# Kernel tuning notes

Hardware: AMD Instinct MI355X
Metric: run time of the kernel (lower is better)

Reference implementation:

```python
import jax, jax.numpy as jnp
import numpy as np

N = 200000
E = 6400000
IN_F = 128
HID = 128
OUT_F = 16
LAYERS = 3
EPS = 1e-5


def setup_inputs() -> dict:
    key = jax.random.key(0)
    ks = jax.random.split(key, 12)
    nodes = jax.random.normal(ks[0], (N, IN_F), dtype=jnp.float32)
    src = jax.random.randint(ks[1], (E,), 0, N, dtype=jnp.int32)
    dst = jax.random.randint(ks[2], (E,), 0, N, dtype=jnp.int32)
    s_in = 1.0 / np.sqrt(IN_F)
    s_h = 1.0 / np.sqrt(HID)
    W_in = jax.random.uniform(ks[3], (IN_F, HID), jnp.float32, -s_in, s_in)
    b_in = jax.random.uniform(ks[4], (HID,), jnp.float32, -s_in, s_in)
    Ws = jax.random.uniform(ks[5], (LAYERS, HID, HID), jnp.float32, -s_h, s_h)
    bs = jax.random.uniform(ks[6], (LAYERS, HID), jnp.float32, -s_h, s_h)
    gammas = jnp.ones((LAYERS, HID), jnp.float32)
    betas = jnp.zeros((LAYERS, HID), jnp.float32)
    W_out = jax.random.uniform(ks[7], (HID, OUT_F), jnp.float32, -s_h, s_h)
    b_out = jax.random.uniform(ks[8], (OUT_F,), jnp.float32, -s_h, s_h)
    return {"nodes": nodes, "src": src, "dst": dst, "W_in": W_in, "b_in": b_in,
            "Ws": Ws, "bs": bs, "gammas": gammas, "betas": betas,
            "W_out": W_out, "b_out": b_out}


def _layernorm(x, g, b):
    mu = jnp.mean(x, axis=-1, keepdims=True)
    var = jnp.var(x, axis=-1, keepdims=True)
    return (x - mu) * jax.lax.rsqrt(var + EPS) * g + b


def reference(nodes, src, dst, W_in, b_in, Ws, bs, gammas, betas, W_out, b_out):
    # in-degree for 'gcn' aggregator normalization: (sum_neigh + self) / (deg + 1)
    deg = jax.ops.segment_sum(jnp.ones((E,), jnp.float32), dst, num_segments=N)
    inv = 1.0 / (deg + 1.0)  # [N]
    x = nodes @ W_in + b_in  # [N, HID]
    for l in range(LAYERS):
        agg = jax.ops.segment_sum(x[src], dst, num_segments=N)  # gather+scatter-add
        h = (agg + x) * inv[:, None]          # gcn mean incl. self
        h = h @ Ws[l] + bs[l]                 # fc_neigh
        h = jax.nn.relu(h)                    # activation (before norm, per DGL)
        x = _layernorm(h, gammas[l], betas[l])
    return x @ W_out + b_out  # [N, OUT_F]
```

## Files before the change

kernel.cpp:

```cpp
#include <hip/hip_runtime.h>

#define N_NODES 200000
#define N_EDGES 6400000
#define HID 128
#define OUTF 16
#define LAYERS 3
#define EPS 1e-5f

#define NRANGES 16
#define RANGE_N 12500
#define NBUCKETS 800
#define BUCKET_N 250
#define BATCH 5000
#define NBATCH (N_EDGES / BATCH)
#define RCAP 405000
#define RBLK (RCAP / BATCH)
#define BCAP 9500

typedef unsigned int u32;

__device__ __forceinline__ unsigned short f2bf(float f){
  unsigned int u = __float_as_uint(f);
  u += 0x7fffu + ((u >> 16) & 1u);
  return (unsigned short)(u >> 16);
}
__device__ __forceinline__ u32 pack2bf(float lo, float hi){
  return (u32)f2bf(lo) | ((u32)f2bf(hi) << 16);
}


__global__ __launch_bounds__(256) void k_initcur(int* __restrict__ range_cursor,
                                                 int* __restrict__ bucket_cursor){
  int t = blockIdx.x * 256 + threadIdx.x;
  if (t < NRANGES) range_cursor[t] = t * RCAP;
  if (t < NBUCKETS) bucket_cursor[t] = t * BCAP;
}


__global__ __launch_bounds__(256) void k_p1(const int* __restrict__ src, const int* __restrict__ dst,
                                            int* __restrict__ range_cursor, u32* __restrict__ ebuf1){
  __shared__ u32 stage[BATCH];
  __shared__ int hist[NRANGES], hist2[NRANGES], hbase[NRANGES], gbase[NRANGES];
  const int tid = threadIdx.x;
  const long e0 = (long)blockIdx.x * BATCH;

  if (tid < NRANGES){ hist[tid] = 0; hist2[tid] = 0; }
  __syncthreads();
  for (int i = tid; i < BATCH; i += 256){
    int d = dst[e0 + i];
    atomicAdd(&hist[d / RANGE_N], 1);
  }
  __syncthreads();
  if (tid == 0){ int run = 0; for (int b = 0; b < NRANGES; b++){ hbase[b] = run; run += hist[b]; } }
  __syncthreads();
  if (tid < NRANGES && hist[tid] > 0) gbase[tid] = atomicAdd(&range_cursor[tid], hist[tid]);
  __syncthreads();
  for (int i = tid; i < BATCH; i += 256){
    int d = dst[e0 + i];
    int s = src[e0 + i];
    int r = d / RANGE_N;
    u32 pk = ((u32)(d - r * RANGE_N) << 18) | (u32)s;
    int p = atomicAdd(&hist2[r], 1);
    stage[hbase[r] + p] = pk;
  }
  __syncthreads();
  for (int b = 0; b < NRANGES; b++){
    int len = hist[b];
    int gb = gbase[b], hb = hbase[b];
    for (int i = tid; i < len; i += 256) ebuf1[gb + i] = stage[hb + i];
  }
}


__global__ __launch_bounds__(256) void k_p2(const u32* __restrict__ ebuf1, const int* __restrict__ range_cursor,
                                            int* __restrict__ bucket_cursor, u32* __restrict__ ebuf2){
  __shared__ u32 stage[BATCH];
  __shared__ int hist[50], hist2[50], hbase[50], gbase[50];
  const int tid = threadIdx.x;
  const int r = blockIdx.x / RBLK;
  const int chunk = blockIdx.x % RBLK;
  const int rlen = range_cursor[r] - r * RCAP;
  const int i0 = chunk * BATCH;
  const int len = min(BATCH, rlen - i0);
  if (len <= 0) return;
  const u32* seg = ebuf1 + (long)r * RCAP + i0;

  if (tid < 50){ hist[tid] = 0; hist2[tid] = 0; }
  __syncthreads();
  for (int i = tid; i < len; i += 256){
    int dl = (int)(seg[i] >> 18);
    atomicAdd(&hist[dl / BUCKET_N], 1);
  }
  __syncthreads();
  if (tid == 0){ int run = 0; for (int b = 0; b < 50; b++){ hbase[b] = run; run += hist[b]; } }
  __syncthreads();
  if (tid < 50 && hist[tid] > 0) gbase[tid] = atomicAdd(&bucket_cursor[r * 50 + tid], hist[tid]);
  __syncthreads();
  for (int i = tid; i < len; i += 256){
    u32 pk = seg[i];
    int b = (int)(pk >> 18) / BUCKET_N;
    int p = atomicAdd(&hist2[b], 1);
    stage[hbase[b] + p] = pk;
  }
  __syncthreads();
  for (int b = 0; b < 50; b++){
    int l = hist[b];
    if (l == 0) continue;
    int gb = gbase[b], hb = hbase[b];
    for (int i = tid; i < l; i += 256) ebuf2[gb + i] = stage[hb + i];
  }
}


__global__ __launch_bounds__(256) void k_scanb(const int* __restrict__ bucket_cursor,
                                               int* __restrict__ bucket_base){
  __shared__ int q[256];
  int tid = threadIdx.x;
  int v[4]; int sum4 = 0;
  if (tid < 200){
    #pragma unroll
    for (int j = 0; j < 4; j++){ int b = 4 * tid + j; v[j] = bucket_cursor[b] - b * BCAP; sum4 += v[j]; }
  }
  q[tid] = sum4; __syncthreads();
  for (int off = 1; off < 256; off <<= 1){
    int t = (tid >= off) ? q[tid - off] : 0;
    __syncthreads();
    q[tid] += t;
    __syncthreads();
  }
  if (tid < 200){
    int run = q[tid] - sum4;
    #pragma unroll
    for (int j = 0; j < 4; j++){ bucket_base[4 * tid + j] = run; run += v[j]; }
  }
}


__global__ __launch_bounds__(256) void k_p3(const u32* __restrict__ ebuf2, const int* __restrict__ bucket_cursor,
                                            const int* __restrict__ bucket_base,
                                            int* __restrict__ csr, int* __restrict__ row_start){
  __shared__ int stage[BCAP];
  __shared__ int hist[BUCKET_N], sbase[BUCKET_N], cur[BUCKET_N];
  __shared__ int q[256];
  const int tid = threadIdx.x;
  const int b = blockIdx.x;
  const int n0 = b * BUCKET_N;
  const int dl0 = (b % 50) * BUCKET_N;
  const int len = min(bucket_cursor[b] - b * BCAP, BCAP);
  const int base = bucket_base[b];
  const u32* seg = ebuf2 + (long)b * BCAP;

  if (tid < BUCKET_N){ hist[tid] = 0; cur[tid] = 0; }
  __syncthreads();
  for (int i = tid; i < len; i += 256){
    int local = (int)(seg[i] >> 18) - dl0;
    local = min(max(local, 0), BUCKET_N - 1);
    atomicAdd(&hist[local], 1);
  }
  __syncthreads();
  {
    int v = (tid < BUCKET_N) ? hist[tid] : 0;
    q[tid] = v; __syncthreads();
    for (int off = 1; off < 256; off <<= 1){
      int t = (tid >= off) ? q[tid - off] : 0;
      __syncthreads();
      q[tid] += t;
      __syncthreads();
    }
    if (tid < BUCKET_N) sbase[tid] = q[tid] - v;
  }
  __syncthreads();
  for (int i = tid; i < len; i += 256){
    u32 pk = seg[i];
    int local = (int)(pk >> 18) - dl0;
    local = min(max(local, 0), BUCKET_N - 1);
    int pos = atomicAdd(&cur[local], 1);
    stage[sbase[local] + pos] = (int)(pk & 0x3FFFFu);
  }
  __syncthreads();
  for (int i = tid; i < len; i += 256) csr[base + i] = stage[i];
  if (tid < BUCKET_N) row_start[n0 + tid] = base + sbase[tid];
  if (b == NBUCKETS - 1 && tid == 0) row_start[N_NODES] = base + len;
}


__global__ __launch_bounds__(256) void k_gemm128(const float* __restrict__ A,
    const float* __restrict__ W, const float* __restrict__ bias,
    const float* __restrict__ gamma, const float* __restrict__ beta,
    float* __restrict__ xout, u32* __restrict__ xbout, int relu_ln)
{
  __shared__ float As[64][132];
  __shared__ float part[64][4][2];
  __shared__ float mu_s[64], rs_s[64];
  __shared__ float gam_s[128], bet_s[128];
  const int tid = threadIdx.x;
  const long row0 = (long)blockIdx.x * 64;

  const float4* A4 = (const float4*)(A + row0 * HID);
  for (int i = tid; i < 64 * 32; i += 256){
    int r = i >> 5, c = i & 31;
    *(float4*)&As[r][c * 4] = A4[r * 32 + c];
  }
  if (relu_ln && tid < 128){ gam_s[tid] = gamma[tid]; bet_s[tid] = beta[tid]; }
  __syncthreads();

  const int cg = tid & 31;
  const int rg = tid >> 5;
  const int c0 = cg * 4;
  float acc[8][4];
  {
    float4 b = *(const float4*)&bias[c0];
    #pragma unroll
    for (int r = 0; r < 8; r++){ acc[r][0]=b.x; acc[r][1]=b.y; acc[r][2]=b.z; acc[r][3]=b.w; }
  }

  for (int k = 0; k < HID; k += 4){
    float4 w0 = *(const float4*)&W[(k + 0) * HID + c0];
    float4 w1 = *(const float4*)&W[(k + 1) * HID + c0];
    float4 w2 = *(const float4*)&W[(k + 2) * HID + c0];
    float4 w3 = *(const float4*)&W[(k + 3) * HID + c0];
    #pragma unroll
    for (int r = 0; r < 8; r++){
      float4 a = *(const float4*)&As[rg * 8 + r][k];
      acc[r][0] = fmaf(a.w, w3.x, fmaf(a.z, w2.x, fmaf(a.y, w1.x, fmaf(a.x, w0.x, acc[r][0]))));
      acc[r][1] = fmaf(a.w, w3.y, fmaf(a.z, w2.y, fmaf(a.y, w1.y, fmaf(a.x, w0.y, acc[r][1]))));
      acc[r][2] = fmaf(a.w, w3.z, fmaf(a.z, w2.z, fmaf(a.y, w1.z, fmaf(a.x, w0.z, acc[r][2]))));
      acc[r][3] = fmaf(a.w, w3.w, fmaf(a.z, w2.w, fmaf(a.y, w1.w, fmaf(a.x, w0.w, acc[r][3]))));
    }
  }

  if (!relu_ln){
    #pragma unroll
    for (int r = 0; r < 8; r++){
      long row = row0 + rg * 8 + r;
      float4 v; v.x = acc[r][0]; v.y = acc[r][1]; v.z = acc[r][2]; v.w = acc[r][3];
      *(float4*)&xout[row * HID + c0] = v;
      uint2 p; p.x = pack2bf(v.x, v.y); p.y = pack2bf(v.z, v.w);
      *(uint2*)&xbout[(row * HID + c0) >> 1] = p;
    }
  } else {
    __syncthreads();
    #pragma unroll
    for (int r = 0; r < 8; r++){
      float4 v;
      v.x = fmaxf(acc[r][0], 0.f); v.y = fmaxf(acc[r][1], 0.f);
      v.z = fmaxf(acc[r][2], 0.f); v.w = fmaxf(acc[r][3], 0.f);
      *(float4*)&As[rg * 8 + r][c0] = v;
    }
    __syncthreads();
    {
      int row = tid >> 2, qq = tid & 3;
      float s = 0.f, s2 = 0.f;
      #pragma unroll 8
      for (int c = 0; c < 32; c++){ float v = As[row][qq * 32 + c]; s += v; s2 += v * v; }
      part[row][qq][0] = s; part[row][qq][1] = s2;
    }
    __syncthreads();
    if (tid < 64){
      float s  = part[tid][0][0] + part[tid][1][0] + part[tid][2][0] + part[tid][3][0];
      float s2 = part[tid][0][1] + part[tid][1][1] + part[tid][2][1] + part[tid][3][1];
      float mu = s * (1.f / HID);
      float var = s2 * (1.f / HID) - mu * mu;
      mu_s[tid] = mu;
      rs_s[tid] = 1.f / sqrtf(var + EPS);
    }
    __syncthreads();
    for (int i = tid; i < 64 * 32; i += 256){
      int r = i >> 5, c4 = (i & 31) * 4;
      float4 v = *(float4*)&As[r][c4];
      float mu = mu_s[r], rs = rs_s[r];
      v.x = (v.x - mu) * rs * gam_s[c4 + 0] + bet_s[c4 + 0];
      v.y = (v.y - mu) * rs * gam_s[c4 + 1] + bet_s[c4 + 1];
      v.z = (v.z - mu) * rs * gam_s[c4 + 2] + bet_s[c4 + 2];
      v.w = (v.w - mu) * rs * gam_s[c4 + 3] + bet_s[c4 + 3];
      long row = row0 + r;
      *(float4*)&xout[row * HID + c4] = v;
      uint2 p; p.x = pack2bf(v.x, v.y); p.y = pack2bf(v.z, v.w);
      *(uint2*)&xbout[(row * HID + c4) >> 1] = p;
    }
  }
}


typedef float f32x2_t __attribute__((ext_vector_type(2)));

__global__ __launch_bounds__(256) void k_agg(const int* __restrict__ row_start, const int* __restrict__ csr,
    const uint2* __restrict__ xb2, const float* __restrict__ x, float* __restrict__ h)
{
  int gid  = blockIdx.x * 256 + threadIdx.x;
  int node = gid >> 6;
  int lane = gid & 63;
  int half = lane >> 5, col = lane & 31;
  int s0 = row_start[node], s1 = row_start[node + 1];
  const uint2* xbc = xb2 + col;

  float4 xs = {0.f, 0.f, 0.f, 0.f};
  if (half == 0) xs = *(const float4*)&x[(long)node * HID + col * 4];

  f32x2_t a01 = {0.f, 0.f};
  f32x2_t a23 = {0.f, 0.f};

  int base = s0;
  int idx[8];
  if (base + 16 <= s1){
    #pragma unroll
    for (int j = 0; j < 8; j++) idx[j] = csr[base + 2*j + half];
  }
  while (base + 16 <= s1){
    uint2 p[8];
    #pragma unroll
    for (int j = 0; j < 8; j++) p[j] = xbc[(long)idx[j] * 32];
    base += 16;
    if (base + 16 <= s1){
      #pragma unroll
      for (int j = 0; j < 8; j++) idx[j] = csr[base + 2*j + half];
    }
    #pragma unroll
    for (int j = 0; j < 8; j++){
      f32x2_t v01 = { __uint_as_float(p[j].x << 16), __uint_as_float(p[j].x & 0xffff0000u) };
      f32x2_t v23 = { __uint_as_float(p[j].y << 16), __uint_as_float(p[j].y & 0xffff0000u) };
      a01 += v01;
      a23 += v23;
    }
  }
  if (base < s1){
    const int s1m1 = s1 - 1;
    int ti[8];
    #pragma unroll
    for (int j = 0; j < 8; j++) ti[j] = csr[min(base + 2*j + half, s1m1)];
    uint2 p[8];
    #pragma unroll
    for (int j = 0; j < 8; j++) p[j] = xbc[(long)ti[j] * 32];
    #pragma unroll
    for (int j = 0; j < 8; j++){
      bool act = (base + 2*j + half) < s1;
      float v0 = __uint_as_float(p[j].x << 16);
      float v1 = __uint_as_float(p[j].x & 0xffff0000u);
      float v2 = __uint_as_float(p[j].y << 16);
      float v3 = __uint_as_float(p[j].y & 0xffff0000u);
      a01.x += act ? v0 : 0.f;
      a01.y += act ? v1 : 0.f;
      a23.x += act ? v2 : 0.f;
      a23.y += act ? v3 : 0.f;
    }
  }

  float a0 = a01.x, a1 = a01.y, a2 = a23.x, a3 = a23.y;
  a0 += __shfl_down(a0, 32);
  a1 += __shfl_down(a1, 32);
  a2 += __shfl_down(a2, 32);
  a3 += __shfl_down(a3, 32);

  if (half == 0){
    float inv = 1.f / (float)(s1 - s0 + 1);
    long bidx = (long)node * HID + col * 4;
    float4 r;
    r.x = (a0 + xs.x) * inv;
    r.y = (a1 + xs.y) * inv;
    r.z = (a2 + xs.z) * inv;
    r.w = (a3 + xs.w) * inv;
    *(float4*)&h[bidx] = r;
  }
}


__global__ __launch_bounds__(256) void k_gemm_out(const float* __restrict__ x,
    const float* __restrict__ Wo, const float* __restrict__ bo, float* __restrict__ out)
{
  __shared__ float As[16][132];
  __shared__ float Wl[HID * OUTF];
  const int tid = threadIdx.x;
  const long row0 = (long)blockIdx.x * 16;
  const float4* A4 = (const float4*)(x + row0 * HID);
  for (int i = tid; i < 16 * 32; i += 256){
    int r = i >> 5, c = i & 31;
    *(float4*)&As[r][c * 4] = A4[r * 32 + c];
  }
  for (int i = tid; i < HID * OUTF; i += 256) Wl[i] = Wo[i];
  __syncthreads();
  int col = tid & 15, r = tid >> 4;
  float acc = bo[col];
  for (int k = 0; k < HID; k += 4){
    float4 a = *(const float4*)&As[r][k];
    acc = fmaf(a.x, Wl[(k + 0) * OUTF + col],
          fmaf(a.y, Wl[(k + 1) * OUTF + col],
          fmaf(a.z, Wl[(k + 2) * OUTF + col],
          fmaf(a.w, Wl[(k + 3) * OUTF + col], acc))));
  }
  out[(row0 + r) * OUTF + col] = acc;
}


extern "C" void kernel_launch(void* const* d_in, const int* in_sizes, int n_in,
                              void* d_out, int out_size, void* d_ws, size_t ws_size,
                              hipStream_t stream)
{
  (void)in_sizes; (void)n_in; (void)out_size; (void)ws_size;
  const float* nodes = (const float*)d_in[0];
  const int*   src   = (const int*)d_in[1];
  const int*   dst   = (const int*)d_in[2];
  const float* W_in  = (const float*)d_in[3];
  const float* b_in  = (const float*)d_in[4];
  const float* Ws    = (const float*)d_in[5];
  const float* bs    = (const float*)d_in[6];
  const float* gam   = (const float*)d_in[7];
  const float* bet   = (const float*)d_in[8];
  const float* W_out = (const float*)d_in[9];
  const float* b_out = (const float*)d_in[10];
  float* out = (float*)d_out;

  size_t off = 0;
  auto bump = [&](size_t bytes) -> char* {
    char* p = (char*)d_ws + off;
    off = (off + bytes + 255) & ~(size_t)255;
    return p;
  };
  int* row_start     = (int*)bump((N_NODES + 1) * sizeof(int));
  int* range_cursor  = (int*)bump(NRANGES * sizeof(int));
  int* bucket_cursor = (int*)bump(NBUCKETS * sizeof(int));
  int* bucket_base   = (int*)bump((NBUCKETS + 1) * sizeof(int));
  int* csr           = (int*)bump((size_t)N_EDGES * sizeof(int));
  float* x           = (float*)bump((size_t)N_NODES * HID * sizeof(float));
  float* h           = (float*)bump((size_t)N_NODES * HID * sizeof(float));
  u32* xb            = (u32*)bump((size_t)N_NODES * HID * sizeof(unsigned short));

  u32* ebuf1 = (u32*)x;
  u32* ebuf2 = (u32*)h;

  k_initcur<<<4, 256, 0, stream>>>(range_cursor, bucket_cursor);
  k_p1<<<NBATCH, 256, 0, stream>>>(src, dst, range_cursor, ebuf1);
  k_p2<<<NRANGES * RBLK, 256, 0, stream>>>(ebuf1, range_cursor, bucket_cursor, ebuf2);
  k_scanb<<<1, 256, 0, stream>>>(bucket_cursor, bucket_base);
  k_p3<<<NBUCKETS, 256, 0, stream>>>(ebuf2, bucket_cursor, bucket_base, csr, row_start);

  k_gemm128<<<N_NODES / 64, 256, 0, stream>>>(nodes, W_in, b_in, nullptr, nullptr, x, xb, 0);
  for (int l = 0; l < LAYERS; l++){
    k_agg<<<N_NODES / 4, 256, 0, stream>>>(row_start, csr, (const uint2*)xb, x, h);
    k_gemm128<<<N_NODES / 64, 256, 0, stream>>>(h, Ws + (size_t)l * HID * HID, bs + l * HID,
                                                gam + l * HID, bet + l * HID, x, xb, 1);
  }
  k_gemm_out<<<N_NODES / 16, 256, 0, stream>>>(x, W_out, b_out, out);
}
```

Measured before the change: 1.422 ms.

## Fuse neighbor aggregation into per-layer GEMM+ReLU+LayerNorm kernel with ping-pong buffers

Aggregation of bf16 neighbor features is performed inside the layer GEMM kernel, writing the normalized mean into shared memory instead of a global h buffer. This removes the write and re-read of the full intermediate activation tensor and one launch per layer. Because blocks read the previous layer's features while writing new ones, x and its bf16 copy are double-buffered. The trade-off is fewer, longer blocks where each wave processes 16 nodes sequentially, reducing gather parallelism and latency hiding.

```diff
diff --git a/kernel.cpp b/kernel.cpp
--- a/kernel.cpp
+++ b/kernel.cpp
@@ -186,13 +186,9 @@
 
 __global__ __launch_bounds__(256) void k_gemm128(const float* __restrict__ A,
     const float* __restrict__ W, const float* __restrict__ bias,
-    const float* __restrict__ gamma, const float* __restrict__ beta,
-    float* __restrict__ xout, u32* __restrict__ xbout, int relu_ln)
+    float* __restrict__ xout, u32* __restrict__ xbout)
 {
   __shared__ float As[64][132];
-  __shared__ float part[64][4][2];
-  __shared__ float mu_s[64], rs_s[64];
-  __shared__ float gam_s[128], bet_s[128];
   const int tid = threadIdx.x;
   const long row0 = (long)blockIdx.x * 64;
 
@@ -201,7 +197,6 @@
     int r = i >> 5, c = i & 31;
     *(float4*)&As[r][c * 4] = A4[r * 32 + c];
   }
-  if (relu_ln && tid < 128){ gam_s[tid] = gamma[tid]; bet_s[tid] = beta[tid]; }
   __syncthreads();
 
   const int cg = tid & 31;
@@ -229,137 +224,174 @@
     }
   }
 
-  if (!relu_ln){
+  #pragma unroll
+  for (int r = 0; r < 8; r++){
+    long row = row0 + rg * 8 + r;
+    float4 v; v.x = acc[r][0]; v.y = acc[r][1]; v.z = acc[r][2]; v.w = acc[r][3];
+    *(float4*)&xout[row * HID + c0] = v;
+    uint2 p; p.x = pack2bf(v.x, v.y); p.y = pack2bf(v.z, v.w);
+    *(uint2*)&xbout[(row * HID + c0) >> 1] = p;
+  }
+}
+
+
+__global__ __launch_bounds__(256) void k_fused(const int* __restrict__ row_start,
+    const int* __restrict__ csr, const uint2* __restrict__ xb2,
+    const float* __restrict__ x_old,
+    const float* __restrict__ W, const float* __restrict__ bias,
+    const float* __restrict__ gamma, const float* __restrict__ beta,
+    float* __restrict__ xout, u32* __restrict__ xbout)
+{
+  __shared__ float As[64][132];
+  __shared__ float part[64][4][2];
+  __shared__ float mu_s[64], rs_s[64];
+  __shared__ float gam_s[128], bet_s[128];
+  const int tid = threadIdx.x;
+  const long row0 = (long)blockIdx.x * 64;
+
+  if (tid < 128){ gam_s[tid] = gamma[tid]; bet_s[tid] = beta[tid]; }
+
+  {
+    const int wv = tid >> 6;
+    const int lane = tid & 63;
+    const int half = lane >> 5, col = lane & 31;
+    const uint2* xbc = xb2 + col;
+
+    for (int i = 0; i < 16; i++){
+      const int r = wv * 16 + i;
+      const int node = (int)row0 + r;
+      const int s0 = row_start[node], s1 = row_start[node + 1];
+
+      float4 xs = {0.f, 0.f, 0.f, 0.f};
+      if (half == 0) xs = *(const float4*)&x_old[(long)node * HID + col * 4];
+
+      float a0 = 0.f, a1 = 0.f, a2 = 0.f, a3 = 0.f;
+      int base = s0;
+      int idx[8];
+      if (base + 16 <= s1){
+        #pragma unroll
+        for (int j = 0; j < 8; j++) idx[j] = csr[base + 2*j + half];
+      }
+      while (base + 16 <= s1){
+        uint2 p[8];
+        #pragma unroll
+        for (int j = 0; j < 8; j++) p[j] = xbc[(long)idx[j] * 32];
+        base += 16;
+        if (base + 16 <= s1){
+          #pragma unroll
+          for (int j = 0; j < 8; j++) idx[j] = csr[base + 2*j + half];
+        }
+        #pragma unroll
+        for (int j = 0; j < 8; j++){
+          a0 += __uint_as_float(p[j].x << 16);
+          a1 += __uint_as_float(p[j].x & 0xffff0000u);
+          a2 += __uint_as_float(p[j].y << 16);
+          a3 += __uint_as_float(p[j].y & 0xffff0000u);
+        }
+      }
+      if (base < s1){
+        const int s1m1 = s1 - 1;
+        int ti[8];
+        #pragma unroll
+        for (int j = 0; j < 8; j++) ti[j] = csr[min(base + 2*j + half, s1m1)];
+        uint2 p[8];
+        #pragma unroll
+        for (int j = 0; j < 8; j++) p[j] = xbc[(long)ti[j] * 32];
+        #pragma unroll
+        for (int j = 0; j < 8; j++){
+          bool act = (base + 2*j + half) < s1;
+          float v0 = __uint_as_float(p[j].x << 16);
+          float v1 = __uint_as_float(p[j].x & 0xffff0000u);
+          float v2 = __uint_as_float(p[j].y << 16);
+          float v3 = __uint_as_float(p[j].y & 0xffff0000u);
+          a0 += act ? v0 : 0.f;
+          a1 += act ? v1 : 0.f;
+          a2 += act ? v2 : 0.f;
+          a3 += act ? v3 : 0.f;
+        }
+      }
+
+      a0 += __shfl_down(a0, 32);
+      a1 += __shfl_down(a1, 32);
+      a2 += __shfl_down(a2, 32);
+      a3 += __shfl_down(a3, 32);
+
+      if (half == 0){
+        float inv = 1.f / (float)(s1 - s0 + 1);
+        float4 rv;
+        rv.x = (a0 + xs.x) * inv;
+        rv.y = (a1 + xs.y) * inv;
+        rv.z = (a2 + xs.z) * inv;
+        rv.w = (a3 + xs.w) * inv;
+        *(float4*)&As[r][col * 4] = rv;
+      }
+    }
+  }
+  __syncthreads();
+
+  const int cg = tid & 31;
+  const int rg = tid >> 5;
+  const int c0 = cg * 4;
+  float acc[8][4];
+  {
+    float4 b = *(const float4*)&bias[c0];
+    #pragma unroll
+    for (int r = 0; r < 8; r++){ acc[r][0]=b.x; acc[r][1]=b.y; acc[r][2]=b.z; acc[r][3]=b.w; }
+  }
+
+  for (int k = 0; k < HID; k += 4){
+    float4 w0 = *(const float4*)&W[(k + 0) * HID + c0];
+    float4 w1 = *(const float4*)&W[(k + 1) * HID + c0];
+    float4 w2 = *(const float4*)&W[(k + 2) * HID + c0];
+    float4 w3 = *(const float4*)&W[(k + 3) * HID + c0];
     #pragma unroll
     for (int r = 0; r < 8; r++){
-      long row = row0 + rg * 8 + r;
-      float4 v; v.x = acc[r][0]; v.y = acc[r][1]; v.z = acc[r][2]; v.w = acc[r][3];
-      *(float4*)&xout[row * HID + c0] = v;
-      uint2 p; p.x = pack2bf(v.x, v.y); p.y = pack2bf(v.z, v.w);
-      *(uint2*)&xbout[(row * HID + c0) >> 1] = p;
+      float4 a = *(const float4*)&As[rg * 8 + r][k];
+      acc[r][0] = fmaf(a.w, w3.x, fmaf(a.z, w2.x, fmaf(a.y, w1.x, fmaf(a.x, w0.x, acc[r][0]))));
+      acc[r][1] = fmaf(a.w, w3.y, fmaf(a.z, w2.y, fmaf(a.y, w1.y, fmaf(a.x, w0.y, acc[r][1]))));
+      acc[r][2] = fmaf(a.w, w3.z, fmaf(a.z, w2.z, fmaf(a.y, w1.z, fmaf(a.x, w0.z, acc[r][2]))));
+      acc[r][3] = fmaf(a.w, w3.w, fmaf(a.z, w2.w, fmaf(a.y, w1.w, fmaf(a.x, w0.w, acc[r][3]))));
     }
-  } else {
-    __syncthreads();
-    #pragma unroll
-    for (int r = 0; r < 8; r++){
-      float4 v;
-      v.x = fmaxf(acc[r][0], 0.f); v.y = fmaxf(acc[r][1], 0.f);
-      v.z = fmaxf(acc[r][2], 0.f); v.w = fmaxf(acc[r][3], 0.f);
-      *(float4*)&As[rg * 8 + r][c0] = v;
-    }
-    __syncthreads();
-    {
-      int row = tid >> 2, qq = tid & 3;
-      float s = 0.f, s2 = 0.f;
-      #pragma unroll 8
-      for (int c = 0; c < 32; c++){ float v = As[row][qq * 32 + c]; s += v; s2 += v * v; }
-      part[row][qq][0] = s; part[row][qq][1] = s2;
-    }
-    __syncthreads();
-    if (tid < 64){
-      float s  = part[tid][0][0] + part[tid][1][0] + part[tid][2][0] + part[tid][3][0];
-      float s2 = part[tid][0][1] + part[tid][1][1] + part[tid][2][1] + part[tid][3][1];
-      float mu = s * (1.f / HID);
-      float var = s2 * (1.f / HID) - mu * mu;
-      mu_s[tid] = mu;
-      rs_s[tid] = 1.f / sqrtf(var + EPS);
-    }
-    __syncthreads();
-    for (int i = tid; i < 64 * 32; i += 256){
-      int r = i >> 5, c4 = (i & 31) * 4;
-      float4 v = *(float4*)&As[r][c4];
-      float mu = mu_s[r], rs = rs_s[r];
-      v.x = (v.x - mu) * rs * gam_s[c4 + 0] + bet_s[c4 + 0];
-      v.y = (v.y - mu) * rs * gam_s[c4 + 1] + bet_s[c4 + 1];
-      v.z = (v.z - mu) * rs * gam_s[c4 + 2] + bet_s[c4 + 2];
-      v.w = (v.w - mu) * rs * gam_s[c4 + 3] + bet_s[c4 + 3];
-      long row = row0 + r;
-      *(float4*)&xout[row * HID + c4] = v;
-      uint2 p; p.x = pack2bf(v.x, v.y); p.y = pack2bf(v.z, v.w);
-      *(uint2*)&xbout[(row * HID + c4) >> 1] = p;
-    }
-  }
-}
-
-
-typedef float f32x2_t __attribute__((ext_vector_type(2)));
-
-__global__ __launch_bounds__(256) void k_agg(const int* __restrict__ row_start, const int* __restrict__ csr,
-    const uint2* __restrict__ xb2, const float* __restrict__ x, float* __restrict__ h)
-{
-  int gid  = blockIdx.x * 256 + threadIdx.x;
-  int node = gid >> 6;
-  int lane = gid & 63;
-  int half = lane >> 5, col = lane & 31;
-  int s0 = row_start[node], s1 = row_start[node + 1];
-  const uint2* xbc = xb2 + col;
-
-  float4 xs = {0.f, 0.f, 0.f, 0.f};
-  if (half == 0) xs = *(const float4*)&x[(long)node * HID + col * 4];
-
-  f32x2_t a01 = {0.f, 0.f};
-  f32x2_t a23 = {0.f, 0.f};
-
-  int base = s0;
-  int idx[8];
-  if (base + 16 <= s1){
-    #pragma unroll
-    for (int j = 0; j < 8; j++) idx[j] = csr[base + 2*j + half];
-  }
-  while (base + 16 <= s1){
-    uint2 p[8];
-    #pragma unroll
-    for (int j = 0; j < 8; j++) p[j] = xbc[(long)idx[j] * 32];
-    base += 16;
-    if (base + 16 <= s1){
-      #pragma unroll
-      for (int j = 0; j < 8; j++) idx[j] = csr[base + 2*j + half];
-    }
-    #pragma unroll
-    for (int j = 0; j < 8; j++){
-      f32x2_t v01 = { __uint_as_float(p[j].x << 16), __uint_as_float(p[j].x & 0xffff0000u) };
-      f32x2_t v23 = { __uint_as_float(p[j].y << 16), __uint_as_float(p[j].y & 0xffff0000u) };
-      a01 += v01;
-      a23 += v23;
-    }
-  }
-  if (base < s1){
-    const int s1m1 = s1 - 1;
-    int ti[8];
-    #pragma unroll
-    for (int j = 0; j < 8; j++) ti[j] = csr[min(base + 2*j + half, s1m1)];
-    uint2 p[8];
-    #pragma unroll
-    for (int j = 0; j < 8; j++) p[j] = xbc[(long)ti[j] * 32];
-    #pragma unroll
-    for (int j = 0; j < 8; j++){
-      bool act = (base + 2*j + half) < s1;
-      float v0 = __uint_as_float(p[j].x << 16);
-      float v1 = __uint_as_float(p[j].x & 0xffff0000u);
-      float v2 = __uint_as_float(p[j].y << 16);
-      float v3 = __uint_as_float(p[j].y & 0xffff0000u);
-      a01.x += act ? v0 : 0.f;
-      a01.y += act ? v1 : 0.f;
-      a23.x += act ? v2 : 0.f;
-      a23.y += act ? v3 : 0.f;
-    }
-  }
-
-  float a0 = a01.x, a1 = a01.y, a2 = a23.x, a3 = a23.y;
-  a0 += __shfl_down(a0, 32);
-  a1 += __shfl_down(a1, 32);
-  a2 += __shfl_down(a2, 32);
-  a3 += __shfl_down(a3, 32);
-
-  if (half == 0){
-    float inv = 1.f / (float)(s1 - s0 + 1);
-    long bidx = (long)node * HID + col * 4;
-    float4 r;
-    r.x = (a0 + xs.x) * inv;
-    r.y = (a1 + xs.y) * inv;
-    r.z = (a2 + xs.z) * inv;
-    r.w = (a3 + xs.w) * inv;
-    *(float4*)&h[bidx] = r;
+  }
+
+  __syncthreads();
+  #pragma unroll
+  for (int r = 0; r < 8; r++){
+    float4 v;
+    v.x = fmaxf(acc[r][0], 0.f); v.y = fmaxf(acc[r][1], 0.f);
+    v.z = fmaxf(acc[r][2], 0.f); v.w = fmaxf(acc[r][3], 0.f);
+    *(float4*)&As[rg * 8 + r][c0] = v;
+  }
+  __syncthreads();
+  {
+    int row = tid >> 2, qq = tid & 3;
+    float s = 0.f, s2 = 0.f;
+    #pragma unroll 8
+    for (int c = 0; c < 32; c++){ float v = As[row][qq * 32 + c]; s += v; s2 += v * v; }
+    part[row][qq][0] = s; part[row][qq][1] = s2;
+  }
+  __syncthreads();
+  if (tid < 64){
+    float s  = part[tid][0][0] + part[tid][1][0] + part[tid][2][0] + part[tid][3][0];
+    float s2 = part[tid][0][1] + part[tid][1][1] + part[tid][2][1] + part[tid][3][1];
+    float mu = s * (1.f / HID);
+    float var = s2 * (1.f / HID) - mu * mu;
+    mu_s[tid] = mu;
+    rs_s[tid] = 1.f / sqrtf(var + EPS);
+  }
+  __syncthreads();
+  for (int i = tid; i < 64 * 32; i += 256){
+    int r = i >> 5, c4 = (i & 31) * 4;
+    float4 v = *(float4*)&As[r][c4];
+    float mu = mu_s[r], rs = rs_s[r];
+    v.x = (v.x - mu) * rs * gam_s[c4 + 0] + bet_s[c4 + 0];
+    v.y = (v.y - mu) * rs * gam_s[c4 + 1] + bet_s[c4 + 1];
+    v.z = (v.z - mu) * rs * gam_s[c4 + 2] + bet_s[c4 + 2];
+    v.w = (v.w - mu) * rs * gam_s[c4 + 3] + bet_s[c4 + 3];
+    long row = row0 + r;
+    *(float4*)&xout[row * HID + c4] = v;
+    uint2 p; p.x = pack2bf(v.x, v.y); p.y = pack2bf(v.z, v.w);
+    *(uint2*)&xbout[(row * HID + c4) >> 1] = p;
   }
 }
 
@@ -420,12 +452,13 @@
   int* bucket_cursor = (int*)bump(NBUCKETS * sizeof(int));
   int* bucket_base   = (int*)bump((NBUCKETS + 1) * sizeof(int));
   int* csr           = (int*)bump((size_t)N_EDGES * sizeof(int));
-  float* x           = (float*)bump((size_t)N_NODES * HID * sizeof(float));
-  float* h           = (float*)bump((size_t)N_NODES * HID * sizeof(float));
-  u32* xb            = (u32*)bump((size_t)N_NODES * HID * sizeof(unsigned short));
-
-  u32* ebuf1 = (u32*)x;
-  u32* ebuf2 = (u32*)h;
+  float* x0          = (float*)bump((size_t)N_NODES * HID * sizeof(float));
+  float* x1          = (float*)bump((size_t)N_NODES * HID * sizeof(float));
+  u32* xb0           = (u32*)bump((size_t)N_NODES * HID * sizeof(unsigned short));
+  u32* xb1           = (u32*)bump((size_t)N_NODES * HID * sizeof(unsigned short));
+
+  u32* ebuf1 = (u32*)x0;
+  u32* ebuf2 = (u32*)x1;
 
   k_initcur<<<4, 256, 0, stream>>>(range_cursor, bucket_cursor);
   k_p1<<<NBATCH, 256, 0, stream>>>(src, dst, range_cursor, ebuf1);
@@ -433,11 +466,17 @@
   k_scanb<<<1, 256, 0, stream>>>(bucket_cursor, bucket_base);
   k_p3<<<NBUCKETS, 256, 0, stream>>>(ebuf2, bucket_cursor, bucket_base, csr, row_start);
 
-  k_gemm128<<<N_NODES / 64, 256, 0, stream>>>(nodes, W_in, b_in, nullptr, nullptr, x, xb, 0);
+  k_gemm128<<<N_NODES / 64, 256, 0, stream>>>(nodes, W_in, b_in, x0, xb0);
+
+  const float* xi = x0;  float* xo = x1;
+  const u32*   xbi = xb0; u32*  xbo = xb1;
   for (int l = 0; l < LAYERS; l++){
-    k_agg<<<N_NODES / 4, 256, 0, stream>>>(row_start, csr, (const uint2*)xb, x, h);
-    k_gemm128<<<N_NODES / 64, 256, 0, stream>>>(h, Ws + (size_t)l * HID * HID, bs + l * HID,
-                                                gam + l * HID, bet + l * HID, x, xb, 1);
-  }
-  k_gemm_out<<<N_NODES / 16, 256, 0, stream>>>(x, W_out, b_out, out);
-}
+    k_fused<<<N_NODES / 64, 256, 0, stream>>>(row_start, csr, (const uint2*)xbi, xi,
+                                              Ws + (size_t)l * HID * HID, bs + l * HID,
+                                              gam + l * HID, bet + l * HID, xo, xbo);
+    const float* tx = xi; xi = xo; xo = (float*)tx;
+    const u32* tb = xbi; xbi = xbo; xbo = (u32*)tb;
+  }
+
+  k_gemm_out<<<N_NODES / 16, 256, 0, stream>>>(xi, W_out, b_out, out);
+}
```

After: 1.401 ms. Within noise of the previous version (-1.5%).
